# Kernel tuning notes

Hardware: AMD Instinct MI355X
Metric: run time of the kernel (lower is better)

## Reference

```python
import jax, jax.numpy as jnp
import numpy as np
import math

PHI = (1 + math.sqrt(5)) / 2
ALPHA = 1 / PHI          # residual scale
BETA = 1 / PHI ** 2      # sparse-matmul scale
DIM = 1910
NZ = int(DIM * DIM / PHI)


def setup_inputs() -> dict:
    key = jax.random.key(0)
    kx, ki, kv = jax.random.split(key, 3)
    x = jax.random.normal(kx, (8, 4096, DIM), dtype=jnp.float32)
    W_indices = jax.random.randint(ki, (2, NZ), 0, DIM, dtype=jnp.int32)
    W_values = jax.random.normal(kv, (NZ,), dtype=jnp.float32) / math.sqrt(DIM)
    return {"x": x, "W_indices": W_indices, "W_values": W_values}


def reference(x, W_indices, W_values):
    dim = x.shape[-1]
    # COO -> dense: duplicate (row,col) entries sum, matching torch.sparse semantics.
    W = jnp.zeros((dim, dim), dtype=x.dtype).at[W_indices[0], W_indices[1]].add(W_values)
    orig_shape = x.shape
    xf = x.reshape(-1, dim)          # [tokens, dim]
    Wx = xf @ W.T                    # (W @ x.T).T == x @ W.T
    out = ALPHA * xf + BETA * Wx
    return out.reshape(orig_shape)
```

## Files before the change

### kernel.cpp

```cpp
#include <hip/hip_runtime.h>
#include <hip/hip_bf16.h>
#include <stdint.h>

#define DIMV 1910
#define KP   1920
#define NT   30
#define TT   120
#define PHI_F  1.6180339887498949f
#define BETA_F 0.3819660112501051f

typedef __attribute__((ext_vector_type(4))) float f32x4;
typedef __attribute__((ext_vector_type(8))) short bf16x8;
typedef __attribute__((ext_vector_type(8))) unsigned short u16x8;

__device__ __forceinline__ void gl16(const void* g, void* l) {
    __builtin_amdgcn_global_load_lds(
        (const __attribute__((address_space(1))) void*)(uintptr_t)g,
        (__attribute__((address_space(3))) void*)(uint32_t)(uintptr_t)l,
        16, 0, 0);
}

__global__ void k_prep(const float* __restrict__ x, unsigned short* __restrict__ xb, int total8,
                       const int* __restrict__ ridx, const int* __restrict__ cidx,
                       const float* __restrict__ vals, float* __restrict__ Wd, int nz) {
    const int tid  = threadIdx.x;
    const int half = (int)gridDim.x >> 1;
    const int b    = (int)blockIdx.x >> 1;
    const int stride = half * 256;
    if ((blockIdx.x & 1) == 0) {
        for (int i = b * 256 + tid; i < total8; i += stride) {
            int v = i * 8;
            int row = v / KP;
            int col = v - row * KP;
            u16x8 o;
            if (col + 8 <= DIMV) {
                const float2* s = (const float2*)(x + (size_t)row * DIMV + col);
                float2 f0 = s[0], f1 = s[1], f2 = s[2], f3 = s[3];
                float f[8] = {f0.x, f0.y, f1.x, f1.y, f2.x, f2.y, f3.x, f3.y};
#pragma unroll
                for (int j = 0; j < 8; ++j) {
                    __hip_bfloat16 bb = __float2bfloat16(f[j]);
                    o[j] = *reinterpret_cast<unsigned short*>(&bb);
                }
            } else {
#pragma unroll
                for (int j = 0; j < 8; ++j) {
                    int c = col + j;
                    float fv = (c < DIMV) ? x[(size_t)row * DIMV + c] : 0.f;
                    __hip_bfloat16 bb = __float2bfloat16(fv);
                    o[j] = *reinterpret_cast<unsigned short*>(&bb);
                }
            }
            *(u16x8*)(xb + (size_t)v) = o;
        }
    } else {
        for (int i = b * 256 + tid; i < nz; i += stride)
            atomicAdd(Wd + (size_t)ridx[i] * DIMV + cidx[i], vals[i]);
    }
}

__global__ void k_build_w(const float* __restrict__ Wd, unsigned short* __restrict__ Wb, int total8) {
    int stride = gridDim.x * blockDim.x;
    for (int i = blockIdx.x * blockDim.x + threadIdx.x; i < total8; i += stride) {
        int v = i * 8;
        int n = v / KP;
        int k = v - n * KP;
        u16x8 o;
#pragma unroll
        for (int j = 0; j < 8; ++j) {
            int kk = k + j;
            float fv = (n < DIMV && kk < DIMV) ? Wd[(size_t)n * DIMV + kk] : 0.f;
            if (kk == n && n < DIMV) fv += PHI_F;
            __hip_bfloat16 b = __float2bfloat16(fv);
            o[j] = *reinterpret_cast<unsigned short*>(&b);
        }
        *(u16x8*)(Wb + (size_t)v) = o;
    }
}

__global__ __launch_bounds__(512, 2) void k_gemm(const short* __restrict__ A,
                                                 const short* __restrict__ B,
                                                 float* __restrict__ C) {
    __shared__ char lds[163840];

    const int bid = blockIdx.x;
    const int bmg = bid & 31;
    const int bn  = bid >> 5;

    const int tid = threadIdx.x;
    const int w   = tid >> 6;
    const int l   = tid & 63;
    const int wm  = w >> 2;
    const int wn  = w & 3;
    const int fr  = l & 15;
    const int q   = l >> 4;

    const int    srow = tid >> 3;
    const size_t KPB  = (size_t)KP * 2;
    const int    swz  = ((tid & 7) ^ (srow & 7)) * 16;
    const char*  bSrc = (const char*)B + (size_t)(bn * 256 + srow) * KPB + swz;
    const size_t sweep = (size_t)64 * KPB;
    char* stDst = lds + tid * 16;

    const int co0  = ((q    ) ^ (fr & 7)) * 16;
    const int co1  = ((4 + q) ^ (fr & 7)) * 16;
    const int aOff = (wm * 128 + fr) * 128;
    const int bOff = (wn * 64 + fr) * 128;

    f32x4 acc[8][4] = {};

#define STAGE_A(src, kk_, dstoff, s) gl16((src) + (size_t)(s) * sweep + (size_t)(kk_) * 128, stDst + (dstoff) + (s) * 8192)
#define STAGE_B(kk_, dstoff, s)      gl16(bSrc  + (size_t)(s) * sweep + (size_t)(kk_) * 128, stDst + 98304 + (dstoff) + (s) * 8192)

    const char* aSrc0 = (const char*)A + (size_t)(bmg * 256 + srow) * KPB + swz;
    const size_t mstep = (size_t)8192 * KPB;

#pragma unroll
    for (int s = 0; s < 4; ++s) STAGE_A(aSrc0, 0, 0, s);
#pragma unroll
    for (int s = 0; s < 4; ++s) STAGE_B(0, 0, s);
#pragma unroll
    for (int s = 0; s < 4; ++s) STAGE_A(aSrc0, 1, 32768, s);
    asm volatile("s_waitcnt vmcnt(4)" ::: "memory");
    __builtin_amdgcn_s_barrier();
    asm volatile("" ::: "memory");

    int boA = 0, stA = 65536;
    int boB = 0, stB = 32768;
    int tkR = 0;
    int kb1 = 1;
    int ka2 = 2;
    int mtR = 0;
    const char* aStage = aSrc0;

    for (int t = 0; t < TT; ++t) {
        const char* pa = lds + boA + aOff;
        const char* pb = lds + 98304 + boB + bOff;
        const bool stb = (t + 1 < TT);
        const bool sta = (t + 2 < TT);
        bf16x8 a[4][2], b0[2][2], b1[2][2];

#pragma unroll
        for (int mi = 0; mi < 4; ++mi) {
            a[mi][0] = *(const bf16x8*)(pa + mi * 2048 + co0);
            a[mi][1] = *(const bf16x8*)(pa + mi * 2048 + co1);
        }
#pragma unroll
        for (int ni = 0; ni < 2; ++ni) {
            b0[ni][0] = *(const bf16x8*)(pb + ni * 2048 + co0);
            b0[ni][1] = *(const bf16x8*)(pb + ni * 2048 + co1);
        }
        if (stb) { STAGE_B(kb1, stB, 0); STAGE_B(kb1, stB, 1); }
        asm volatile("" ::: "memory");
        __builtin_amdgcn_s_barrier();
        asm volatile("s_waitcnt lgkmcnt(0)" ::: "memory");
        __builtin_amdgcn_s_setprio(1);
#pragma unroll
        for (int kk = 0; kk < 2; ++kk)
#pragma unroll
            for (int mi = 0; mi < 4; ++mi)
#pragma unroll
                for (int ni = 0; ni < 2; ++ni)
                    acc[mi][ni] = __builtin_amdgcn_mfma_f32_16x16x32_bf16(a[mi][kk], b0[ni][kk], acc[mi][ni], 0, 0, 0);
        __builtin_amdgcn_s_setprio(0);
        asm volatile("" ::: "memory");
        __builtin_amdgcn_s_barrier();
        asm volatile("" ::: "memory");

#pragma unroll
        for (int ni = 0; ni < 2; ++ni) {
            b1[ni][0] = *(const bf16x8*)(pb + 4096 + ni * 2048 + co0);
            b1[ni][1] = *(const bf16x8*)(pb + 4096 + ni * 2048 + co1);
        }
        if (stb) { STAGE_B(kb1, stB, 2); STAGE_B(kb1, stB, 3); }
        if (sta) { STAGE_A(aStage, ka2, stA, 0); STAGE_A(aStage, ka2, stA, 1); }
        asm volatile("" ::: "memory");
        __builtin_amdgcn_s_barrier();
        asm volatile("s_waitcnt lgkmcnt(0)" ::: "memory");
        __builtin_amdgcn_s_setprio(1);
#pragma unroll
        for (int kk = 0; kk < 2; ++kk)
#pragma unroll
            for (int mi = 0; mi < 4; ++mi)
#pragma unroll
                for (int ni = 0; ni < 2; ++ni)
                    acc[mi][ni + 2] = __builtin_amdgcn_mfma_f32_16x16x32_bf16(a[mi][kk], b1[ni][kk], acc[mi][ni + 2], 0, 0, 0);
        __builtin_amdgcn_s_setprio(0);
        asm volatile("" ::: "memory");
        __builtin_amdgcn_s_barrier();
        asm volatile("" ::: "memory");

#pragma unroll
        for (int mi = 0; mi < 4; ++mi) {
            a[mi][0] = *(const bf16x8*)(pa + 8192 + mi * 2048 + co0);
            a[mi][1] = *(const bf16x8*)(pa + 8192 + mi * 2048 + co1);
        }
        if (sta) { STAGE_A(aStage, ka2, stA, 2); STAGE_A(aStage, ka2, stA, 3); }
        asm volatile("" ::: "memory");
        __builtin_amdgcn_s_barrier();
        asm volatile("s_waitcnt lgkmcnt(0)" ::: "memory");
        __builtin_amdgcn_s_setprio(1);
#pragma unroll
        for (int kk = 0; kk < 2; ++kk)
#pragma unroll
            for (int mi = 0; mi < 4; ++mi)
#pragma unroll
                for (int ni = 0; ni < 2; ++ni)
                    acc[mi + 4][ni + 2] = __builtin_amdgcn_mfma_f32_16x16x32_bf16(a[mi][kk], b1[ni][kk], acc[mi + 4][ni + 2], 0, 0, 0);
#pragma unroll
        for (int kk = 0; kk < 2; ++kk)
#pragma unroll
            for (int mi = 0; mi < 4; ++mi)
#pragma unroll
                for (int ni = 0; ni < 2; ++ni)
                    acc[mi + 4][ni] = __builtin_amdgcn_mfma_f32_16x16x32_bf16(a[mi][kk], b0[ni][kk], acc[mi + 4][ni], 0, 0, 0);
        __builtin_amdgcn_s_setprio(0);
        if (sta) { asm volatile("s_waitcnt vmcnt(4)" ::: "memory"); }
        else     { asm volatile("s_waitcnt vmcnt(0)" ::: "memory"); }
        __builtin_amdgcn_s_barrier();
        asm volatile("" ::: "memory");

        if (tkR == NT - 1) {
            const int bm    = mtR * 32 + bmg;
            const int grow0 = bm * 256 + wm * 128 + q * 4;
            const int gcol0 = bn * 256 + wn * 64 + fr;
#pragma unroll
            for (int ei = 0; ei < 8; ++ei) {
#pragma unroll
                for (int ni = 0; ni < 4; ++ni) {
                    int gcol = gcol0 + ni * 16;
                    if (gcol < DIMV) {
                        size_t base = (size_t)(grow0 + ei * 16) * DIMV + gcol;
#pragma unroll
                        for (int r = 0; r < 4; ++r)
                            C[base + (size_t)r * DIMV] = BETA_F * acc[ei][ni][r];
                    }
                }
            }
            if (t + 1 < TT) {
#pragma unroll
                for (int ei = 0; ei < 8; ++ei)
#pragma unroll
                    for (int ni = 0; ni < 4; ++ni)
                        acc[ei][ni] = (f32x4)(0.f);
            }
            tkR = 0; ++mtR;
        } else ++tkR;

        boA = (boA == 65536) ? 0 : boA + 32768;
        stA = (stA == 65536) ? 0 : stA + 32768;
        boB ^= 32768;
        stB ^= 32768;
        if (++kb1 == NT) kb1 = 0;
        if (++ka2 == NT) { ka2 = 0; aStage += mstep; }
    }
#undef STAGE_A
#undef STAGE_B
}

extern "C" void kernel_launch(void* const* d_in, const int* in_sizes, int n_in,
                              void* d_out, int out_size, void* d_ws, size_t ws_size,
                              hipStream_t stream) {
    const float* x    = (const float*)d_in[0];
    const int*   widx = (const int*)d_in[1];
    const float* wval = (const float*)d_in[2];
    float* out = (float*)d_out;

    const int nz = in_sizes[2];
    const int M  = in_sizes[0] / DIMV;

    const size_t xb_bytes = (size_t)M * KP * 2;
    const size_t wb_bytes = (size_t)2048 * KP * 2;
    const size_t wd_bytes = (size_t)DIMV * DIMV * 4;
    char* ws = (char*)d_ws;
    unsigned short* xb = (unsigned short*)ws;
    unsigned short* Wb = (unsigned short*)(ws + xb_bytes);
    float*          Wd = (float*)(ws + xb_bytes + wb_bytes);
    if (ws_size < xb_bytes + wb_bytes + wd_bytes) return;

    hipMemsetAsync(Wd, 0, wd_bytes, stream);
    k_prep<<<2048, 256, 0, stream>>>(x, xb, M * KP / 8, widx, widx + nz, wval, Wd, nz);
    k_build_w<<<1800, 256, 0, stream>>>(Wd, Wb, KP * KP / 8);
    k_gemm<<<256, 512, 0, stream>>>((const short*)xb, (const short*)Wb, out);
}
```

Baseline: 388.9 us.

## Load GEMM B operand straight from global into registers, skip LDS staging

The weight (B) tile no longer goes through LDS. Each wave loads its own B fragments from global memory into a register double buffer (bCur/bNxt), one k-step ahead. This shrinks LDS from 160KB to 96KB and cuts the four barriers per k-iteration down to one, with A still triple-buffered in LDS. In exchange, B reads become strided 16-byte global loads that rely on cache hits, register pressure rises with the extra 64 VGPRs of B buffers, and the vmcnt accounting now mixes B and A loads.

```diff
diff --git a/kernel.cpp b/kernel.cpp
--- a/kernel.cpp
+++ b/kernel.cpp
@@ -81,7 +81,7 @@
 __global__ __launch_bounds__(512, 2) void k_gemm(const short* __restrict__ A,
                                                  const short* __restrict__ B,
                                                  float* __restrict__ C) {
-    __shared__ char lds[163840];
+    __shared__ char lds[98304];
 
     const int bid = blockIdx.x;
     const int bmg = bid & 31;
@@ -98,19 +98,26 @@
     const int    srow = tid >> 3;
     const size_t KPB  = (size_t)KP * 2;
     const int    swz  = ((tid & 7) ^ (srow & 7)) * 16;
-    const char*  bSrc = (const char*)B + (size_t)(bn * 256 + srow) * KPB + swz;
     const size_t sweep = (size_t)64 * KPB;
     char* stDst = lds + tid * 16;
 
     const int co0  = ((q    ) ^ (fr & 7)) * 16;
     const int co1  = ((4 + q) ^ (fr & 7)) * 16;
     const int aOff = (wm * 128 + fr) * 128;
-    const int bOff = (wn * 64 + fr) * 128;
+
+    const char* bG = (const char*)B + (size_t)(bn * 256 + wn * 64 + fr) * KPB + q * 16;
 
     f32x4 acc[8][4] = {};
+    bf16x8 a[4][2], bCur[4][2], bNxt[4][2];
 
 #define STAGE_A(src, kk_, dstoff, s) gl16((src) + (size_t)(s) * sweep + (size_t)(kk_) * 128, stDst + (dstoff) + (s) * 8192)
-#define STAGE_B(kk_, dstoff, s)      gl16(bSrc  + (size_t)(s) * sweep + (size_t)(kk_) * 128, stDst + 98304 + (dstoff) + (s) * 8192)
+#define LOADB(dst, kt)                                                           \
+    _Pragma("unroll")                                                            \
+    for (int c = 0; c < 4; ++c) {                                                \
+        const char* bp = bG + (size_t)((c >> 1) * 32 + (c & 1) * 16) * KPB + (size_t)(kt) * 128; \
+        dst[c][0] = *(const bf16x8*)(bp);                                        \
+        dst[c][1] = *(const bf16x8*)(bp + 64);                                   \
+    }
 
     const char* aSrc0 = (const char*)A + (size_t)(bmg * 256 + srow) * KPB + swz;
     const size_t mstep = (size_t)8192 * KPB;
@@ -118,15 +125,11 @@
 #pragma unroll
     for (int s = 0; s < 4; ++s) STAGE_A(aSrc0, 0, 0, s);
 #pragma unroll
-    for (int s = 0; s < 4; ++s) STAGE_B(0, 0, s);
-#pragma unroll
     for (int s = 0; s < 4; ++s) STAGE_A(aSrc0, 1, 32768, s);
+    LOADB(bCur, 0)
     asm volatile("s_waitcnt vmcnt(4)" ::: "memory");
-    __builtin_amdgcn_s_barrier();
-    asm volatile("" ::: "memory");
 
     int boA = 0, stA = 65536;
-    int boB = 0, stB = 32768;
     int tkR = 0;
     int kb1 = 1;
     int ka2 = 2;
@@ -134,91 +137,49 @@
     const char* aStage = aSrc0;
 
     for (int t = 0; t < TT; ++t) {
+        asm volatile("" ::: "memory");
+        __builtin_amdgcn_s_barrier();
+        asm volatile("" ::: "memory");
+
         const char* pa = lds + boA + aOff;
-        const char* pb = lds + 98304 + boB + bOff;
         const bool stb = (t + 1 < TT);
         const bool sta = (t + 2 < TT);
-        bf16x8 a[4][2], b0[2][2], b1[2][2];
 
 #pragma unroll
         for (int mi = 0; mi < 4; ++mi) {
             a[mi][0] = *(const bf16x8*)(pa + mi * 2048 + co0);
             a[mi][1] = *(const bf16x8*)(pa + mi * 2048 + co1);
         }
-#pragma unroll
-        for (int ni = 0; ni < 2; ++ni) {
-            b0[ni][0] = *(const bf16x8*)(pb + ni * 2048 + co0);
-            b0[ni][1] = *(const bf16x8*)(pb + ni * 2048 + co1);
-        }
-        if (stb) { STAGE_B(kb1, stB, 0); STAGE_B(kb1, stB, 1); }
-        asm volatile("" ::: "memory");
-        __builtin_amdgcn_s_barrier();
-        asm volatile("s_waitcnt lgkmcnt(0)" ::: "memory");
+        if (stb) { LOADB(bNxt, kb1) }
         __builtin_amdgcn_s_setprio(1);
 #pragma unroll
         for (int kk = 0; kk < 2; ++kk)
 #pragma unroll
             for (int mi = 0; mi < 4; ++mi)
 #pragma unroll
-                for (int ni = 0; ni < 2; ++ni)
-                    acc[mi][ni] = __builtin_amdgcn_mfma_f32_16x16x32_bf16(a[mi][kk], b0[ni][kk], acc[mi][ni], 0, 0, 0);
+                for (int c = 0; c < 4; ++c)
+                    acc[mi][c] = __builtin_amdgcn_mfma_f32_16x16x32_bf16(a[mi][kk], bCur[c][kk], acc[mi][c], 0, 0, 0);
         __builtin_amdgcn_s_setprio(0);
-        asm volatile("" ::: "memory");
-        __builtin_amdgcn_s_barrier();
-        asm volatile("" ::: "memory");
-
-#pragma unroll
-        for (int ni = 0; ni < 2; ++ni) {
-            b1[ni][0] = *(const bf16x8*)(pb + 4096 + ni * 2048 + co0);
-            b1[ni][1] = *(const bf16x8*)(pb + 4096 + ni * 2048 + co1);
-        }
-        if (stb) { STAGE_B(kb1, stB, 2); STAGE_B(kb1, stB, 3); }
-        if (sta) { STAGE_A(aStage, ka2, stA, 0); STAGE_A(aStage, ka2, stA, 1); }
-        asm volatile("" ::: "memory");
-        __builtin_amdgcn_s_barrier();
-        asm volatile("s_waitcnt lgkmcnt(0)" ::: "memory");
-        __builtin_amdgcn_s_setprio(1);
-#pragma unroll
-        for (int kk = 0; kk < 2; ++kk)
-#pragma unroll
-            for (int mi = 0; mi < 4; ++mi)
-#pragma unroll
-                for (int ni = 0; ni < 2; ++ni)
-                    acc[mi][ni + 2] = __builtin_amdgcn_mfma_f32_16x16x32_bf16(a[mi][kk], b1[ni][kk], acc[mi][ni + 2], 0, 0, 0);
-        __builtin_amdgcn_s_setprio(0);
-        asm volatile("" ::: "memory");
-        __builtin_amdgcn_s_barrier();
-        asm volatile("" ::: "memory");
 
 #pragma unroll
         for (int mi = 0; mi < 4; ++mi) {
             a[mi][0] = *(const bf16x8*)(pa + 8192 + mi * 2048 + co0);
             a[mi][1] = *(const bf16x8*)(pa + 8192 + mi * 2048 + co1);
         }
-        if (sta) { STAGE_A(aStage, ka2, stA, 2); STAGE_A(aStage, ka2, stA, 3); }
-        asm volatile("" ::: "memory");
-        __builtin_amdgcn_s_barrier();
-        asm volatile("s_waitcnt lgkmcnt(0)" ::: "memory");
+        if (sta) { STAGE_A(aStage, ka2, stA, 0); STAGE_A(aStage, ka2, stA, 1);
+                   STAGE_A(aStage, ka2, stA, 2); STAGE_A(aStage, ka2, stA, 3); }
         __builtin_amdgcn_s_setprio(1);
 #pragma unroll
         for (int kk = 0; kk < 2; ++kk)
 #pragma unroll
             for (int mi = 0; mi < 4; ++mi)
 #pragma unroll
-                for (int ni = 0; ni < 2; ++ni)
-                    acc[mi + 4][ni + 2] = __builtin_amdgcn_mfma_f32_16x16x32_bf16(a[mi][kk], b1[ni][kk], acc[mi + 4][ni + 2], 0, 0, 0);
-#pragma unroll
-        for (int kk = 0; kk < 2; ++kk)
-#pragma unroll
-            for (int mi = 0; mi < 4; ++mi)
-#pragma unroll
-                for (int ni = 0; ni < 2; ++ni)
-                    acc[mi + 4][ni] = __builtin_amdgcn_mfma_f32_16x16x32_bf16(a[mi][kk], b0[ni][kk], acc[mi + 4][ni], 0, 0, 0);
+                for (int c = 0; c < 4; ++c)
+                    acc[mi + 4][c] = __builtin_amdgcn_mfma_f32_16x16x32_bf16(a[mi][kk], bCur[c][kk], acc[mi + 4][c], 0, 0, 0);
         __builtin_amdgcn_s_setprio(0);
+
         if (sta) { asm volatile("s_waitcnt vmcnt(4)" ::: "memory"); }
         else     { asm volatile("s_waitcnt vmcnt(0)" ::: "memory"); }
-        __builtin_amdgcn_s_barrier();
-        asm volatile("" ::: "memory");
 
         if (tkR == NT - 1) {
             const int bm    = mtR * 32 + bmg;
@@ -247,15 +208,18 @@
             tkR = 0; ++mtR;
         } else ++tkR;
 
+        if (stb) {
+#pragma unroll
+            for (int c = 0; c < 4; ++c) { bCur[c][0] = bNxt[c][0]; bCur[c][1] = bNxt[c][1]; }
+        }
+
         boA = (boA == 65536) ? 0 : boA + 32768;
         stA = (stA == 65536) ? 0 : stA + 32768;
-        boB ^= 32768;
-        stB ^= 32768;
         if (++kb1 == NT) kb1 = 0;
         if (++ka2 == NT) { ka2 = 0; aStage += mstep; }
     }
 #undef STAGE_A
-#undef STAGE_B
+#undef LOADB
 }
 
 extern "C" void kernel_launch(void* const* d_in, const int* in_sizes, int n_in,
```

New measurement: 520.2 us. 33.8% more time.
